# Optimization experiments

Measured on AMD Instinct MI355X. Metric: run time of the kernel, lower is better.

The kernel has to match this reference:

```python
import jax, jax.numpy as jnp
import numpy as np

EPS_PROJ = 0.004   # float32 branch of _project
EPS_MIN = 1e-15


def _poincare_linear(x, weight_v, weight_g, bias, c):
    c = c.reshape(())
    rc = jnp.sqrt(c)
    # z_unit: column-normalized weight (weight_v / ||weight_v||_col)
    z_unit = weight_v / jnp.maximum(jnp.linalg.norm(weight_v, axis=0), EPS_MIN)  # [in, out]
    # unidirectional Poincare MLR
    drcr = 2.0 * rc * bias                                  # [out]
    rcx = rc * x                                            # [N, in]
    cx2 = jnp.sum(rcx * rcx, axis=-1, keepdims=True)        # [N, 1]
    num = 2.0 * (rcx @ z_unit) * jnp.cosh(drcr) - (1.0 + cx2) * jnp.sinh(drcr)
    mlr = 2.0 * weight_g / rc * jnp.arcsinh(num / jnp.maximum(1.0 - cx2, EPS_MIN))  # [N, out]
    # map back to the ball: sinh, then gyro-half map
    y = jnp.sinh(rc * mlr) / rc
    y = y / (1.0 + jnp.sqrt(1.0 + c * jnp.sum(y * y, axis=-1, keepdims=True)))
    # _project onto ball of curvature k = -c
    k = -c
    maxnorm = (1.0 - EPS_PROJ) / jnp.sqrt(jnp.maximum(jnp.abs(k), EPS_MIN))
    maxnorm = jnp.where(k < 0, maxnorm, jnp.float32(1e15))
    norm = jnp.maximum(jnp.linalg.norm(y, axis=-1, keepdims=True), EPS_MIN)
    return jnp.where(norm > maxnorm, y / norm * maxnorm, y)


def setup_inputs() -> dict:
    key = jax.random.key(0)
    k1, k2, k3 = jax.random.split(key, 3)
    N, IN, OUT = 32768, 1024, 1024
    # points strictly inside the unit Poincare ball (||x|| ~ 0.64)
    x = jax.random.normal(k1, (N, IN), dtype=jnp.float32) * 0.02
    std = (2.0 * IN * OUT) ** (-0.5)
    weight_v = jax.random.normal(k2, (IN, OUT), dtype=jnp.float32) * std
    weight_g = jax.random.uniform(k3, (OUT,), dtype=jnp.float32, minval=0.5, maxval=1.5) * std * (IN ** 0.5)
    bias = jnp.zeros((OUT,), dtype=jnp.float32)
    c = jnp.ones((1,), dtype=jnp.float32)
    return {"x": x, "weight_v": weight_v, "weight_g": weight_g, "bias": bias, "c": c}


def reference(x, weight_v, weight_g, bias, c):
    return _poincare_linear(x, weight_v, weight_g, bias, c)
```

## Files before the change

kernel.cpp:

```cpp
#include <hip/hip_runtime.h>

#define K_DIM 1024
#define N_DIM 1024

typedef short v8s __attribute__((ext_vector_type(8)));
typedef float v4f __attribute__((ext_vector_type(4)));

__device__ __forceinline__ unsigned int bf16_rne(float f) {
    unsigned int u = __float_as_uint(f);
    u += 0x7FFFu + ((u >> 16) & 1u);
    return u >> 16;
}

__global__ void sumsq_cols(const float* __restrict__ wv, float* __restrict__ colss) {
    __shared__ float red[4][64];
    const int t = threadIdx.x;
    const int cj = t & 63, rr = t >> 6;
    const int col = (blockIdx.x & 15) * 64 + cj;
    const int k0 = (blockIdx.x >> 4) * 128 + rr * 32;
    float ss = 0.f;
#pragma unroll 8
    for (int i = 0; i < 32; ++i) {
        float v = wv[(size_t)(k0 + i) * N_DIM + col];
        ss = fmaf(v, v, ss);
    }
    red[rr][cj] = ss;
    __syncthreads();
    if (rr == 0) atomicAdd(&colss[col], red[0][cj] + red[1][cj] + red[2][cj] + red[3][cj]);
}

__global__ void finalize_cols(const float* __restrict__ colss, const float* __restrict__ wg,
                              const float* __restrict__ bias, const float* __restrict__ cptr,
                              float* __restrict__ colinv, float* __restrict__ coshd,
                              float* __restrict__ sinhd, float* __restrict__ gfac) {
    const int col = blockIdx.x * 256 + threadIdx.x;
    const float rc = sqrtf(cptr[0]);
    colinv[col] = 1.0f / fmaxf(sqrtf(colss[col]), 1e-15f);
    float d = 2.0f * rc * bias[col];
    float e = __expf(d), ie = 1.0f / e;
    coshd[col] = 0.5f * (e + ie);
    sinhd[col] = 0.5f * (e - ie);
    gfac[col] = 2.0f * wg[col];
}

__global__ void build_bt(const float* __restrict__ wv, const float* __restrict__ colinv,
                         unsigned short* __restrict__ Btf) {
    __shared__ float tile[64 * 65];
    const int t = threadIdx.x;
    const int ti = blockIdx.x & 15;
    const int tj = blockIdx.x >> 4;
    {
        const int kl = t >> 2;
        const int cc = t & 3;
        const float* src = wv + (size_t)(ti * 64 + kl) * N_DIM + tj * 64 + cc * 16;
        float4 fq[4];
#pragma unroll
        for (int i = 0; i < 4; ++i) fq[i] = ((const float4*)src)[i];
        float* dst = &tile[kl * 65 + cc * 16];
#pragma unroll
        for (int i = 0; i < 4; ++i) {
            dst[4 * i + 0] = fq[i].x; dst[4 * i + 1] = fq[i].y;
            dst[4 * i + 2] = fq[i].z; dst[4 * i + 3] = fq[i].w;
        }
    }
    __syncthreads();
    {
        const int nl = t & 63, kc = t >> 6;
        const int n = tj * 64 + nl;
        const float ci = colinv[n];
        const int nt_g = tj * 4 + (nl >> 4);
#pragma unroll
        for (int h = 0; h < 2; ++h) {
            const int k8g = ti * 8 + kc * 2 + h;
            const int ks_g = k8g >> 2;
            const int L = (nl & 15) | ((k8g & 3) << 4);
            unsigned int p[4];
#pragma unroll
            for (int j = 0; j < 4; ++j) {
                float v0 = tile[(kc * 16 + h * 8 + 2 * j) * 65 + nl] * ci;
                float v1 = tile[(kc * 16 + h * 8 + 2 * j + 1) * 65 + nl] * ci;
                p[j] = bf16_rne(v0) | (bf16_rne(v1) << 16);
            }
            *(uint4*)(Btf + ((size_t)(nt_g * 32 + ks_g) * 64 + L) * 8) =
                make_uint4(p[0], p[1], p[2], p[3]);
        }
    }
}

__global__ void prep_a(const float* __restrict__ x, unsigned short* __restrict__ Axf,
                       float* __restrict__ rowss) {
    __shared__ float xs[16 * 1028];
    const int t = threadIdx.x;
    const int b = blockIdx.x;
    {
        const int r = t >> 4;
        const int c = t & 15;
        const float* xp = x + (size_t)(b * 16 + r) * K_DIM + c * 4;
        float* dst = &xs[r * 1028 + c * 4];
        float ss = 0.f;
#pragma unroll
        for (int it = 0; it < 16; ++it) {
            float4 v = *(const float4*)(xp + it * 64);
            ss = fmaf(v.x, v.x, ss); ss = fmaf(v.y, v.y, ss);
            ss = fmaf(v.z, v.z, ss); ss = fmaf(v.w, v.w, ss);
            *(float4*)(dst + it * 64) = v;
        }
        ss += __shfl_xor(ss, 1); ss += __shfl_xor(ss, 2);
        ss += __shfl_xor(ss, 4); ss += __shfl_xor(ss, 8);
        if (c == 0) rowss[b * 16 + r] = ss;
    }
    __syncthreads();
    {
        const int w = t >> 6, L = t & 63;
        const int lm = L & 15, q = L >> 4;
#pragma unroll
        for (int i = 0; i < 8; ++i) {
            const int ks = w * 8 + i;
            const float* src = &xs[lm * 1028 + ks * 32 + q * 8];
            float4 f0 = *(const float4*)(src);
            float4 f1 = *(const float4*)(src + 4);
            float vals[8] = {f0.x, f0.y, f0.z, f0.w, f1.x, f1.y, f1.z, f1.w};
            unsigned int p[4];
#pragma unroll
            for (int j = 0; j < 4; ++j)
                p[j] = bf16_rne(vals[2 * j]) | (bf16_rne(vals[2 * j + 1]) << 16);
            *(uint4*)(Axf + ((size_t)b * 32 + ks) * 512 + L * 8) =
                make_uint4(p[0], p[1], p[2], p[3]);
        }
    }
}

__launch_bounds__(512, 2)
__global__ void gemm_fused(const unsigned short* __restrict__ Axf,
                           const unsigned short* __restrict__ Btf,
                           const float* __restrict__ rowss, const float* __restrict__ cptr,
                           const float* __restrict__ coshd, const float* __restrict__ sinhd,
                           const float* __restrict__ gfac,
                           float* __restrict__ out) {
    __shared__ __align__(16) unsigned short As[4 * 32 * 512];

    const int t = threadIdx.x;
    const int w = t >> 6, L = t & 63;
    const int lm = L & 15, q = L >> 4;
    const int bm = blockIdx.x;
    const int r0 = bm * 64;

    const unsigned short* ag = Axf + (size_t)bm * 65536;
#pragma unroll
    for (int r = 0; r < 16; ++r) {
        __builtin_amdgcn_global_load_lds(
            (const __attribute__((address_space(1))) unsigned int*)(ag + r * 4096 + t * 8),
            (__attribute__((address_space(3))) unsigned int*)(As + r * 4096 + t * 8),
            16, 0, 0);
    }

    const unsigned short* bw = Btf + (size_t)(w * 8) * 32 * 512 + (size_t)L * 8;

    v4f acc[4][8];
#pragma unroll
    for (int i = 0; i < 4; ++i)
#pragma unroll
        for (int j = 0; j < 8; ++j) acc[i][j] = (v4f){0.f, 0.f, 0.f, 0.f};

    v8s bA[8], bB[8];
#pragma unroll
    for (int n = 0; n < 8; ++n)
        bA[n] = *(const v8s*)(bw + (n * 32) * 512);

    __syncthreads();

    const unsigned short* asw = As + L * 8;

#pragma unroll 1
    for (int kp = 0; kp < 16; ++kp) {
        const int k0 = kp * 2;
#pragma unroll
        for (int n = 0; n < 8; ++n)
            bB[n] = *(const v8s*)(bw + (n * 32 + k0 + 1) * 512);
        {
            v8s a[4];
#pragma unroll
            for (int mt = 0; mt < 4; ++mt)
                a[mt] = *(const v8s*)(asw + (mt * 32 + k0) * 512);
            __builtin_amdgcn_s_setprio(1);
#pragma unroll
            for (int mt = 0; mt < 4; ++mt)
#pragma unroll
                for (int n = 0; n < 8; ++n)
                    acc[mt][n] = __builtin_amdgcn_mfma_f32_16x16x32_bf16(
                        a[mt], bA[n], acc[mt][n], 0, 0, 0);
            __builtin_amdgcn_s_setprio(0);
        }
        if (kp < 15) {
#pragma unroll
            for (int n = 0; n < 8; ++n)
                bA[n] = *(const v8s*)(bw + (n * 32 + k0 + 2) * 512);
        }
        {
            v8s a[4];
#pragma unroll
            for (int mt = 0; mt < 4; ++mt)
                a[mt] = *(const v8s*)(asw + (mt * 32 + k0 + 1) * 512);
            __builtin_amdgcn_s_setprio(1);
#pragma unroll
            for (int mt = 0; mt < 4; ++mt)
#pragma unroll
                for (int n = 0; n < 8; ++n)
                    acc[mt][n] = __builtin_amdgcn_mfma_f32_16x16x32_bf16(
                        a[mt], bB[n], acc[mt][n], 0, 0, 0);
            __builtin_amdgcn_s_setprio(0);
        }
    }

    float* s_rsum = (float*)As;

    const float cc = cptr[0];
    const float rc = sqrtf(cc);
    const float two_rc = 2.0f * rc;
    const float halfinvrc = 0.5f / rc;
    float ch[8], sh[8], gf[8];
#pragma unroll
    for (int n = 0; n < 8; ++n) {
        const int col = w * 128 + n * 16 + lm;
        ch[n] = coshd[col]; sh[n] = sinhd[col]; gf[n] = gfac[col];
    }

    __syncthreads();
    if (t < 64) s_rsum[t] = 0.f;
    __syncthreads();

#pragma unroll
    for (int mt = 0; mt < 4; ++mt) {
        const int mloc = mt * 16 + q * 4;
        float sx[4];
#pragma unroll
        for (int rr = 0; rr < 4; ++rr) sx[rr] = cc * rowss[r0 + mloc + rr];
        float rs[4] = {0.f, 0.f, 0.f, 0.f};
#pragma unroll
        for (int n = 0; n < 8; ++n) {
            v4f d = acc[mt][n];
#pragma unroll
            for (int rr = 0; rr < 4; ++rr) {
                float cx2 = sx[rr];
                float num = two_rc * d[rr] * ch[n] - (1.0f + cx2) * sh[n];
                float den = fmaxf(1.0f - cx2, 1e-15f);
                float tt = num * __builtin_amdgcn_rcpf(den);
                float as_ = __logf(fabsf(tt) + sqrtf(fmaf(tt, tt, 1.0f)));
                as_ = copysignf(as_, tt);
                float u = gf[n] * as_;
                float e = __expf(u);
                float y = (e - __builtin_amdgcn_rcpf(e)) * halfinvrc;
                d[rr] = y;
                rs[rr] = fmaf(y, y, rs[rr]);
            }
            acc[mt][n] = d;
        }
#pragma unroll
        for (int rr = 0; rr < 4; ++rr) {
            float v = rs[rr];
            v += __shfl_xor(v, 1); v += __shfl_xor(v, 2);
            v += __shfl_xor(v, 4); v += __shfl_xor(v, 8);
            if (lm == 0) atomicAdd(&s_rsum[mloc + rr], v);
        }
    }
    __syncthreads();

    const float mn = (cc > 0.f) ? 0.996f / sqrtf(fmaxf(cc, 1e-15f)) : 1e15f;
#pragma unroll
    for (int mt = 0; mt < 4; ++mt) {
        const int mloc = mt * 16 + q * 4;
        float f[4];
#pragma unroll
        for (int rr = 0; rr < 4; ++rr) {
            const float s = s_rsum[mloc + rr];
            const float scale = 1.0f / (1.0f + sqrtf(fmaf(cc, s, 1.0f)));
            const float nrm = fmaxf(sqrtf(s) * scale, 1e-15f);
            f[rr] = scale * (nrm > mn ? mn / nrm : 1.0f);
        }
#pragma unroll
        for (int rr = 0; rr < 4; ++rr) {
            float* op = out + (size_t)(r0 + mloc + rr) * N_DIM + w * 128 + lm;
#pragma unroll
            for (int n = 0; n < 8; ++n) op[n * 16] = acc[mt][n][rr] * f[rr];
        }
    }
}

__launch_bounds__(256, 3)
__global__ void gemm_phase(const float* __restrict__ x, const unsigned short* __restrict__ Btf,
                           const float* __restrict__ cptr, const float* __restrict__ coshd,
                           const float* __restrict__ sinhd, const float* __restrict__ gfac,
                           float* __restrict__ out, float* __restrict__ rowsum) {
    __shared__ __align__(16) unsigned short As[16 * 512];
    __shared__ __align__(16) unsigned short Bs[16 * 512];
    __shared__ float s_cx2[128];
    __shared__ float s_rsum[128];

    const int t = threadIdx.x;
    const int w = t >> 6, L = t & 63;
    const int lm = L & 15, q = L >> 4;
    const int bn = blockIdx.x & 7;
    const int bm = blockIdx.x >> 3;
    const int r0 = bm * 128;

    if (t < 128) { s_cx2[t] = 0.f; s_rsum[t] = 0.f; }

    v4f acc[16];
#pragma unroll
    for (int i = 0; i < 16; ++i) acc[i] = (v4f){0.f, 0.f, 0.f, 0.f};

    const int smt0 = w * 2;
    const float* xr0 = x + (size_t)(r0 + smt0 * 16 + lm) * K_DIM;
    const float* xr1 = xr0 + (size_t)16 * K_DIM;
    float xp0 = 0.f, xp1 = 0.f;
    const int wm = w & 1, wn = w >> 1;

    for (int kq = 0; kq < 16; ++kq) {
        const int kbase = kq * 64;
#pragma unroll
        for (int i = 0; i < 4; ++i) {
            const int nt = smt0 + (i & 1);
            const int ks = i >> 1;
            const unsigned short* gp =
                Btf + ((size_t)((bn * 8 + nt) * 32 + (kq * 2 + ks)) * 64 + L) * 8;
            __builtin_amdgcn_global_load_lds(
                (const __attribute__((address_space(1))) unsigned int*)gp,
                (__attribute__((address_space(3))) unsigned int*)&Bs[(nt * 2 + ks) * 512],
                16, 0, 0);
        }
#pragma unroll
        for (int i = 0; i < 4; ++i) {
            const int half = i & 1;
            const int ks = i >> 1;
            const float* xr = half ? xr1 : xr0;
            const int kg = kbase + ks * 32 + q * 8;
            float4 f0 = *(const float4*)(xr + kg);
            float4 f1 = *(const float4*)(xr + kg + 4);
            float vals[8] = {f0.x, f0.y, f0.z, f0.w, f1.x, f1.y, f1.z, f1.w};
            unsigned int pk[4];
            float ssl = 0.f;
#pragma unroll
            for (int j = 0; j < 4; ++j) {
                ssl = fmaf(vals[2 * j], vals[2 * j], ssl);
                ssl = fmaf(vals[2 * j + 1], vals[2 * j + 1], ssl);
                pk[j] = bf16_rne(vals[2 * j]) | (bf16_rne(vals[2 * j + 1]) << 16);
            }
            if (half) xp1 += ssl; else xp0 += ssl;
            *(uint4*)&As[((smt0 + half) * 2 + ks) * 512 + L * 8] =
                make_uint4(pk[0], pk[1], pk[2], pk[3]);
        }
        __syncthreads();
#pragma unroll
        for (int ks = 0; ks < 2; ++ks) {
            v8s a[4], b[4];
#pragma unroll
            for (int mi = 0; mi < 4; ++mi)
                a[mi] = *(const v8s*)&As[((wm * 4 + mi) * 2 + ks) * 512 + L * 8];
#pragma unroll
            for (int ni = 0; ni < 4; ++ni)
                b[ni] = *(const v8s*)&Bs[((wn * 4 + ni) * 2 + ks) * 512 + L * 8];
#pragma unroll
            for (int mi = 0; mi < 4; ++mi)
#pragma unroll
                for (int ni = 0; ni < 4; ++ni)
                    acc[mi * 4 + ni] = __builtin_amdgcn_mfma_f32_16x16x32_bf16(
                        a[mi], b[ni], acc[mi * 4 + ni], 0, 0, 0);
        }
        __syncthreads();
    }

    atomicAdd(&s_cx2[smt0 * 16 + lm], xp0);
    atomicAdd(&s_cx2[smt0 * 16 + 16 + lm], xp1);
    __syncthreads();

    const float cc = cptr[0];
    const float rc = sqrtf(cc);
    const float two_rc = 2.0f * rc;
    const float halfinvrc = 0.5f / rc;
    float ch[4], sh[4], gf[4];
#pragma unroll
    for (int ni = 0; ni < 4; ++ni) {
        const int n = bn * 128 + wn * 64 + ni * 16 + lm;
        ch[ni] = coshd[n]; sh[ni] = sinhd[n]; gf[ni] = gfac[n];
    }
#pragma unroll
    for (int mi = 0; mi < 4; ++mi) {
        const int mloc = wm * 64 + mi * 16 + q * 4;
        float sx[4];
#pragma unroll
        for (int rr = 0; rr < 4; ++rr) sx[rr] = cc * s_cx2[mloc + rr];
        float rs[4] = {0.f, 0.f, 0.f, 0.f};
#pragma unroll
        for (int ni = 0; ni < 4; ++ni) {
            v4f d = acc[mi * 4 + ni];
#pragma unroll
            for (int rr = 0; rr < 4; ++rr) {
                float cx2 = sx[rr];
                float num = two_rc * d[rr] * ch[ni] - (1.0f + cx2) * sh[ni];
                float den = fmaxf(1.0f - cx2, 1e-15f);
                float tt = num * __builtin_amdgcn_rcpf(den);
                float as_ = __logf(fabsf(tt) + sqrtf(fmaf(tt, tt, 1.0f)));
                as_ = copysignf(as_, tt);
                float u = gf[ni] * as_;
                float e = __expf(u);
                float y = (e - __builtin_amdgcn_rcpf(e)) * halfinvrc;
                d[rr] = y;
                rs[rr] = fmaf(y, y, rs[rr]);
            }
            acc[mi * 4 + ni] = d;
        }
#pragma unroll
        for (int rr = 0; rr < 4; ++rr) {
            float v = rs[rr];
            v += __shfl_xor(v, 1); v += __shfl_xor(v, 2);
            v += __shfl_xor(v, 4); v += __shfl_xor(v, 8);
            if (lm == 0) atomicAdd(&s_rsum[mloc + rr], v);
        }
#pragma unroll
        for (int rr = 0; rr < 4; ++rr) {
            const int row = r0 + mloc + rr;
            float* op = out + (size_t)row * N_DIM + bn * 128 + wn * 64 + lm;
#pragma unroll
            for (int ni = 0; ni < 4; ++ni) op[ni * 16] = acc[mi * 4 + ni][rr];
        }
    }
    __syncthreads();
    if (t < 128) atomicAdd(&rowsum[r0 + t], s_rsum[t]);
}

__global__ void rescale(float* __restrict__ out, const float* __restrict__ rowsum,
                        const float* __restrict__ cptr) {
    const int t = threadIdx.x;
    const int row = blockIdx.x * 4 + (t >> 6);
    const float cc = cptr[0];
    const float s = rowsum[row];
    const float scale = 1.0f / (1.0f + sqrtf(fmaf(cc, s, 1.0f)));
    const float nrm = fmaxf(sqrtf(s) * scale, 1e-15f);
    const float mn = (cc > 0.f) ? 0.996f / sqrtf(fmaxf(cc, 1e-15f)) : 1e15f;
    const float f = scale * (nrm > mn ? mn / nrm : 1.0f);
    float4* p = (float4*)(out + (size_t)row * N_DIM) + (t & 63);
#pragma unroll
    for (int j = 0; j < 4; ++j) {
        float4 v = p[j * 64];
        v.x *= f; v.y *= f; v.z *= f; v.w *= f;
        p[j * 64] = v;
    }
}

extern "C" void kernel_launch(void* const* d_in, const int* in_sizes, int n_in,
                              void* d_out, int out_size, void* d_ws, size_t ws_size,
                              hipStream_t stream) {
    const float* x    = (const float*)d_in[0];
    const float* wv   = (const float*)d_in[1];
    const float* wg   = (const float*)d_in[2];
    const float* bias = (const float*)d_in[3];
    const float* cptr = (const float*)d_in[4];
    float* out = (float*)d_out;

    const int OUT = in_sizes[2];
    const int IN  = in_sizes[1] / OUT;
    const int M   = in_sizes[0] / IN;

    float* colss  = (float*)d_ws;
    float* rowsum = colss + 1024;
    float* rowss  = rowsum + M;
    float* colinv = rowss + M;
    float* coshd  = colinv + 1024;
    float* sinhd  = coshd + 1024;
    float* gfac   = sinhd + 1024;
    unsigned short* Btf = (unsigned short*)(gfac + 1024);
    unsigned short* Axf = Btf + (size_t)IN * OUT;

    const size_t need = (size_t)(1024 + 2 * M + 4096) * 4 + (size_t)IN * OUT * 2
                      + (size_t)M * IN * 2;

    hipMemsetAsync(colss, 0, 1024 * sizeof(float), stream);
    sumsq_cols<<<128, 256, 0, stream>>>(wv, colss);
    finalize_cols<<<OUT / 256, 256, 0, stream>>>(colss, wg, bias, cptr, colinv, coshd, sinhd, gfac);
    build_bt<<<(IN / 64) * (OUT / 64), 256, 0, stream>>>(wv, colinv, Btf);
    if (ws_size >= need) {
        prep_a<<<M / 16, 256, 0, stream>>>(x, Axf, rowss);
        gemm_fused<<<M / 64, 512, 0, stream>>>(
            Axf, Btf, rowss, cptr, coshd, sinhd, gfac, out);
    } else {
        hipMemsetAsync(rowsum, 0, (size_t)M * sizeof(float), stream);
        gemm_phase<<<(M / 128) * (OUT / 128), 256, 0, stream>>>(
            x, Btf, cptr, coshd, sinhd, gfac, out, rowsum);
        rescale<<<M / 4, 256, 0, stream>>>(out, rowsum, cptr);
    }
}
```

Baseline: 362.3 us.

## Fuse x bf16 conversion into persistent GEMM and merge weight prep kernels

Drops the separate prep_a pass that wrote a bf16 copy of x to global memory. The GEMM becomes a persistent kernel over 256 blocks that converts each 64-row x panel to bf16 straight into an XOR-swizzled LDS layout, accumulating row sums of squares in shared memory. The next panel's staging overlaps with the current panel's epilogue. The three weight-prep kernels (column norms, finalize, transpose) merge into one prep_w kernel that recomputes column sums per block, which adds redundant reads of weight_v. The fallback path, memsets and global atomics are removed.

```diff
diff --git a/kernel.cpp b/kernel.cpp
--- a/kernel.cpp
+++ b/kernel.cpp
@@ -2,6 +2,7 @@
 
 #define K_DIM 1024
 #define N_DIM 1024
+#define GRID 256
 
 typedef short v8s __attribute__((ext_vector_type(8)));
 typedef float v4f __attribute__((ext_vector_type(4)));
@@ -12,51 +13,34 @@
     return u >> 16;
 }
 
-__global__ void sumsq_cols(const float* __restrict__ wv, float* __restrict__ colss) {
-    __shared__ float red[4][64];
-    const int t = threadIdx.x;
-    const int cj = t & 63, rr = t >> 6;
-    const int col = (blockIdx.x & 15) * 64 + cj;
-    const int k0 = (blockIdx.x >> 4) * 128 + rr * 32;
-    float ss = 0.f;
-#pragma unroll 8
-    for (int i = 0; i < 32; ++i) {
-        float v = wv[(size_t)(k0 + i) * N_DIM + col];
-        ss = fmaf(v, v, ss);
-    }
-    red[rr][cj] = ss;
-    __syncthreads();
-    if (rr == 0) atomicAdd(&colss[col], red[0][cj] + red[1][cj] + red[2][cj] + red[3][cj]);
-}
-
-__global__ void finalize_cols(const float* __restrict__ colss, const float* __restrict__ wg,
-                              const float* __restrict__ bias, const float* __restrict__ cptr,
-                              float* __restrict__ colinv, float* __restrict__ coshd,
-                              float* __restrict__ sinhd, float* __restrict__ gfac) {
-    const int col = blockIdx.x * 256 + threadIdx.x;
-    const float rc = sqrtf(cptr[0]);
-    colinv[col] = 1.0f / fmaxf(sqrtf(colss[col]), 1e-15f);
-    float d = 2.0f * rc * bias[col];
-    float e = __expf(d), ie = 1.0f / e;
-    coshd[col] = 0.5f * (e + ie);
-    sinhd[col] = 0.5f * (e - ie);
-    gfac[col] = 2.0f * wg[col];
-}
-
-__global__ void build_bt(const float* __restrict__ wv, const float* __restrict__ colinv,
-                         unsigned short* __restrict__ Btf) {
+__global__ void prep_w(const float* __restrict__ wv, const float* __restrict__ wg,
+                       const float* __restrict__ bias, const float* __restrict__ cptr,
+                       float* __restrict__ coshd, float* __restrict__ sinhd,
+                       float* __restrict__ gfac, unsigned short* __restrict__ Btf) {
     __shared__ float tile[64 * 65];
+    __shared__ float cred[4][64];
+    __shared__ float cinv[64];
     const int t = threadIdx.x;
     const int ti = blockIdx.x & 15;
     const int tj = blockIdx.x >> 4;
     {
-        const int kl = t >> 2;
-        const int cc = t & 3;
-        const float* src = wv + (size_t)(ti * 64 + kl) * N_DIM + tj * 64 + cc * 16;
+        const int cj = t & 63, rg = t >> 6;
+        const float* wp = wv + (size_t)(rg * 256) * N_DIM + tj * 64 + cj;
+        float ss = 0.f;
+#pragma unroll 4
+        for (int r = 0; r < 256; ++r) {
+            float v = wp[(size_t)r * N_DIM];
+            ss = fmaf(v, v, ss);
+        }
+        cred[rg][cj] = ss;
+    }
+    {
+        const int kl = t >> 2, cq = t & 3;
+        const float* src = wv + (size_t)(ti * 64 + kl) * N_DIM + tj * 64 + cq * 16;
         float4 fq[4];
 #pragma unroll
         for (int i = 0; i < 4; ++i) fq[i] = ((const float4*)src)[i];
-        float* dst = &tile[kl * 65 + cc * 16];
+        float* dst = &tile[kl * 65 + cq * 16];
 #pragma unroll
         for (int i = 0; i < 4; ++i) {
             dst[4 * i + 0] = fq[i].x; dst[4 * i + 1] = fq[i].y;
@@ -64,10 +48,23 @@
         }
     }
     __syncthreads();
+    if (t < 64) {
+        float s = cred[0][t] + cred[1][t] + cred[2][t] + cred[3][t];
+        cinv[t] = 1.0f / fmaxf(sqrtf(s), 1e-15f);
+        if (ti == 0) {
+            const int col = tj * 64 + t;
+            const float rc = sqrtf(cptr[0]);
+            float d = 2.0f * rc * bias[col];
+            float e = __expf(d), ie = 1.0f / e;
+            coshd[col] = 0.5f * (e + ie);
+            sinhd[col] = 0.5f * (e - ie);
+            gfac[col] = 2.0f * wg[col];
+        }
+    }
+    __syncthreads();
     {
         const int nl = t & 63, kc = t >> 6;
-        const int n = tj * 64 + nl;
-        const float ci = colinv[n];
+        const float ci = cinv[nl];
         const int nt_g = tj * 4 + (nl >> 4);
 #pragma unroll
         for (int h = 0; h < 2; ++h) {
@@ -87,137 +84,55 @@
     }
 }
 
-__global__ void prep_a(const float* __restrict__ x, unsigned short* __restrict__ Axf,
-                       float* __restrict__ rowss) {
-    __shared__ float xs[16 * 1028];
-    const int t = threadIdx.x;
-    const int b = blockIdx.x;
-    {
-        const int r = t >> 4;
-        const int c = t & 15;
-        const float* xp = x + (size_t)(b * 16 + r) * K_DIM + c * 4;
-        float* dst = &xs[r * 1028 + c * 4];
+__device__ __forceinline__ void stage_panel(const float* __restrict__ xp,
+                                            unsigned short* __restrict__ Asl,
+                                            float* __restrict__ rowssbuf, int t) {
+#pragma unroll 2
+    for (int it = 0; it < 16; ++it) {
+        const int g = it * 512 + t;
+        const int row = g >> 7, k8 = g & 127;
+        const float4* fp = (const float4*)xp + (size_t)g * 2;
+        float4 f0 = fp[0];
+        float4 f1 = fp[1];
+        float vals[8] = {f0.x, f0.y, f0.z, f0.w, f1.x, f1.y, f1.z, f1.w};
+        unsigned int p[4];
         float ss = 0.f;
 #pragma unroll
-        for (int it = 0; it < 16; ++it) {
-            float4 v = *(const float4*)(xp + it * 64);
-            ss = fmaf(v.x, v.x, ss); ss = fmaf(v.y, v.y, ss);
-            ss = fmaf(v.z, v.z, ss); ss = fmaf(v.w, v.w, ss);
-            *(float4*)(dst + it * 64) = v;
-        }
-        ss += __shfl_xor(ss, 1); ss += __shfl_xor(ss, 2);
-        ss += __shfl_xor(ss, 4); ss += __shfl_xor(ss, 8);
-        if (c == 0) rowss[b * 16 + r] = ss;
-    }
-    __syncthreads();
-    {
-        const int w = t >> 6, L = t & 63;
-        const int lm = L & 15, q = L >> 4;
-#pragma unroll
-        for (int i = 0; i < 8; ++i) {
-            const int ks = w * 8 + i;
-            const float* src = &xs[lm * 1028 + ks * 32 + q * 8];
-            float4 f0 = *(const float4*)(src);
-            float4 f1 = *(const float4*)(src + 4);
-            float vals[8] = {f0.x, f0.y, f0.z, f0.w, f1.x, f1.y, f1.z, f1.w};
-            unsigned int p[4];
-#pragma unroll
-            for (int j = 0; j < 4; ++j)
-                p[j] = bf16_rne(vals[2 * j]) | (bf16_rne(vals[2 * j + 1]) << 16);
-            *(uint4*)(Axf + ((size_t)b * 32 + ks) * 512 + L * 8) =
-                make_uint4(p[0], p[1], p[2], p[3]);
-        }
+        for (int j = 0; j < 4; ++j) {
+            ss = fmaf(vals[2 * j], vals[2 * j], ss);
+            ss = fmaf(vals[2 * j + 1], vals[2 * j + 1], ss);
+            p[j] = bf16_rne(vals[2 * j]) | (bf16_rne(vals[2 * j + 1]) << 16);
+        }
+        ss += __shfl_xor(ss, 1);  ss += __shfl_xor(ss, 2);  ss += __shfl_xor(ss, 4);
+        ss += __shfl_xor(ss, 8);  ss += __shfl_xor(ss, 16); ss += __shfl_xor(ss, 32);
+        if ((t & 63) == 0) atomicAdd(&rowssbuf[row], ss);
+        const int mt = row >> 4, lm2 = row & 15, ks = k8 >> 2, qq = k8 & 3;
+        const int idx = ((mt * 32 + ks) * 512) + (((lm2 ^ (ks & 7)) | (qq << 4)) * 8);
+        *(uint4*)&Asl[idx] = make_uint4(p[0], p[1], p[2], p[3]);
     }
 }
 
 __launch_bounds__(512, 2)
-__global__ void gemm_fused(const unsigned short* __restrict__ Axf,
+__global__ void gemm_fused(const float* __restrict__ x,
                            const unsigned short* __restrict__ Btf,
-                           const float* __restrict__ rowss, const float* __restrict__ cptr,
+                           const float* __restrict__ cptr,
                            const float* __restrict__ coshd, const float* __restrict__ sinhd,
                            const float* __restrict__ gfac,
-                           float* __restrict__ out) {
+                           float* __restrict__ out, int panels) {
     __shared__ __align__(16) unsigned short As[4 * 32 * 512];
+    __shared__ float s_rowss[2][64];
+    __shared__ float s_rsum[64];
 
     const int t = threadIdx.x;
     const int w = t >> 6, L = t & 63;
     const int lm = L & 15, q = L >> 4;
     const int bm = blockIdx.x;
-    const int r0 = bm * 64;
-
-    const unsigned short* ag = Axf + (size_t)bm * 65536;
-#pragma unroll
-    for (int r = 0; r < 16; ++r) {
-        __builtin_amdgcn_global_load_lds(
-            (const __attribute__((address_space(1))) unsigned int*)(ag + r * 4096 + t * 8),
-            (__attribute__((address_space(3))) unsigned int*)(As + r * 4096 + t * 8),
-            16, 0, 0);
-    }
-
-    const unsigned short* bw = Btf + (size_t)(w * 8) * 32 * 512 + (size_t)L * 8;
-
-    v4f acc[4][8];
-#pragma unroll
-    for (int i = 0; i < 4; ++i)
-#pragma unroll
-        for (int j = 0; j < 8; ++j) acc[i][j] = (v4f){0.f, 0.f, 0.f, 0.f};
-
-    v8s bA[8], bB[8];
-#pragma unroll
-    for (int n = 0; n < 8; ++n)
-        bA[n] = *(const v8s*)(bw + (n * 32) * 512);
-
-    __syncthreads();
-
-    const unsigned short* asw = As + L * 8;
-
-#pragma unroll 1
-    for (int kp = 0; kp < 16; ++kp) {
-        const int k0 = kp * 2;
-#pragma unroll
-        for (int n = 0; n < 8; ++n)
-            bB[n] = *(const v8s*)(bw + (n * 32 + k0 + 1) * 512);
-        {
-            v8s a[4];
-#pragma unroll
-            for (int mt = 0; mt < 4; ++mt)
-                a[mt] = *(const v8s*)(asw + (mt * 32 + k0) * 512);
-            __builtin_amdgcn_s_setprio(1);
-#pragma unroll
-            for (int mt = 0; mt < 4; ++mt)
-#pragma unroll
-                for (int n = 0; n < 8; ++n)
-                    acc[mt][n] = __builtin_amdgcn_mfma_f32_16x16x32_bf16(
-                        a[mt], bA[n], acc[mt][n], 0, 0, 0);
-            __builtin_amdgcn_s_setprio(0);
-        }
-        if (kp < 15) {
-#pragma unroll
-            for (int n = 0; n < 8; ++n)
-                bA[n] = *(const v8s*)(bw + (n * 32 + k0 + 2) * 512);
-        }
-        {
-            v8s a[4];
-#pragma unroll
-            for (int mt = 0; mt < 4; ++mt)
-                a[mt] = *(const v8s*)(asw + (mt * 32 + k0 + 1) * 512);
-            __builtin_amdgcn_s_setprio(1);
-#pragma unroll
-            for (int mt = 0; mt < 4; ++mt)
-#pragma unroll
-                for (int n = 0; n < 8; ++n)
-                    acc[mt][n] = __builtin_amdgcn_mfma_f32_16x16x32_bf16(
-                        a[mt], bB[n], acc[mt][n], 0, 0, 0);
-            __builtin_amdgcn_s_setprio(0);
-        }
-    }
-
-    float* s_rsum = (float*)As;
 
     const float cc = cptr[0];
     const float rc = sqrtf(cc);
     const float two_rc = 2.0f * rc;
     const float halfinvrc = 0.5f / rc;
+    const float mn = (cc > 0.f) ? 0.996f / sqrtf(fmaxf(cc, 1e-15f)) : 1e15f;
     float ch[8], sh[8], gf[8];
 #pragma unroll
     for (int n = 0; n < 8; ++n) {
@@ -225,225 +140,134 @@
         ch[n] = coshd[col]; sh[n] = sinhd[col]; gf[n] = gfac[col];
     }
 
+    const unsigned short* bw = Btf + (size_t)(w * 8) * 32 * 512 + (size_t)L * 8;
+
+    if (t < 64) s_rowss[0][t] = 0.f;
     __syncthreads();
-    if (t < 64) s_rsum[t] = 0.f;
-    __syncthreads();
-
-#pragma unroll
-    for (int mt = 0; mt < 4; ++mt) {
-        const int mloc = mt * 16 + q * 4;
-        float sx[4];
-#pragma unroll
-        for (int rr = 0; rr < 4; ++rr) sx[rr] = cc * rowss[r0 + mloc + rr];
-        float rs[4] = {0.f, 0.f, 0.f, 0.f};
-#pragma unroll
-        for (int n = 0; n < 8; ++n) {
-            v4f d = acc[mt][n];
+    stage_panel(x + (size_t)bm * 64 * K_DIM, As, s_rowss[0], t);
+
+#pragma unroll 1
+    for (int i = 0; i < panels; ++i) {
+        const int p = bm + i * GRID;
+        const int pb = i & 1, nb = pb ^ 1;
+        const bool more = (i + 1 < panels);
+        __syncthreads();
+
+        v4f acc[4][8];
+#pragma unroll
+        for (int a = 0; a < 4; ++a)
+#pragma unroll
+            for (int b = 0; b < 8; ++b) acc[a][b] = (v4f){0.f, 0.f, 0.f, 0.f};
+
+        v8s bA[8], bB[8];
+#pragma unroll
+        for (int n = 0; n < 8; ++n)
+            bA[n] = *(const v8s*)(bw + (n * 32) * 512);
+
+#pragma unroll 1
+        for (int kp = 0; kp < 16; ++kp) {
+            const int k0 = kp * 2;
+#pragma unroll
+            for (int n = 0; n < 8; ++n)
+                bB[n] = *(const v8s*)(bw + (n * 32 + k0 + 1) * 512);
+            {
+                const int lx = ((lm ^ (k0 & 7)) | (q << 4)) * 8;
+                v8s a[4];
+#pragma unroll
+                for (int mt = 0; mt < 4; ++mt)
+                    a[mt] = *(const v8s*)&As[(mt * 32 + k0) * 512 + lx];
+                __builtin_amdgcn_s_setprio(1);
+#pragma unroll
+                for (int mt = 0; mt < 4; ++mt)
+#pragma unroll
+                    for (int n = 0; n < 8; ++n)
+                        acc[mt][n] = __builtin_amdgcn_mfma_f32_16x16x32_bf16(
+                            a[mt], bA[n], acc[mt][n], 0, 0, 0);
+                __builtin_amdgcn_s_setprio(0);
+            }
+            if (kp < 15) {
+#pragma unroll
+                for (int n = 0; n < 8; ++n)
+                    bA[n] = *(const v8s*)(bw + (n * 32 + k0 + 2) * 512);
+            }
+            {
+                const int lx = ((lm ^ ((k0 + 1) & 7)) | (q << 4)) * 8;
+                v8s a[4];
+#pragma unroll
+                for (int mt = 0; mt < 4; ++mt)
+                    a[mt] = *(const v8s*)&As[(mt * 32 + k0 + 1) * 512 + lx];
+                __builtin_amdgcn_s_setprio(1);
+#pragma unroll
+                for (int mt = 0; mt < 4; ++mt)
+#pragma unroll
+                    for (int n = 0; n < 8; ++n)
+                        acc[mt][n] = __builtin_amdgcn_mfma_f32_16x16x32_bf16(
+                            a[mt], bB[n], acc[mt][n], 0, 0, 0);
+                __builtin_amdgcn_s_setprio(0);
+            }
+        }
+
+        __syncthreads();
+        if (t < 64) { s_rsum[t] = 0.f; if (more) s_rowss[nb][t] = 0.f; }
+        __syncthreads();
+
+        if (more) stage_panel(x + (size_t)(p + GRID) * 64 * K_DIM, As, s_rowss[nb], t);
+
+        const float* rb = s_rowss[pb];
+#pragma unroll
+        for (int mt = 0; mt < 4; ++mt) {
+            const int mloc = mt * 16 + q * 4;
+            float sx[4];
+#pragma unroll
+            for (int rr = 0; rr < 4; ++rr) sx[rr] = cc * rb[mloc + rr];
+            float rs[4] = {0.f, 0.f, 0.f, 0.f};
+#pragma unroll
+            for (int n = 0; n < 8; ++n) {
+                v4f d = acc[mt][n];
+#pragma unroll
+                for (int rr = 0; rr < 4; ++rr) {
+                    float cx2 = sx[rr];
+                    float num = two_rc * d[rr] * ch[n] - (1.0f + cx2) * sh[n];
+                    float den = fmaxf(1.0f - cx2, 1e-15f);
+                    float tt = num * __builtin_amdgcn_rcpf(den);
+                    float as_ = __logf(fabsf(tt) + sqrtf(fmaf(tt, tt, 1.0f)));
+                    as_ = copysignf(as_, tt);
+                    float u = gf[n] * as_;
+                    float e = __expf(u);
+                    float y = (e - __builtin_amdgcn_rcpf(e)) * halfinvrc;
+                    d[rr] = y;
+                    rs[rr] = fmaf(y, y, rs[rr]);
+                }
+                acc[mt][n] = d;
+            }
 #pragma unroll
             for (int rr = 0; rr < 4; ++rr) {
-                float cx2 = sx[rr];
-                float num = two_rc * d[rr] * ch[n] - (1.0f + cx2) * sh[n];
-                float den = fmaxf(1.0f - cx2, 1e-15f);
-                float tt = num * __builtin_amdgcn_rcpf(den);
-                float as_ = __logf(fabsf(tt) + sqrtf(fmaf(tt, tt, 1.0f)));
-                as_ = copysignf(as_, tt);
-                float u = gf[n] * as_;
-                float e = __expf(u);
-                float y = (e - __builtin_amdgcn_rcpf(e)) * halfinvrc;
-                d[rr] = y;
-                rs[rr] = fmaf(y, y, rs[rr]);
-            }
-            acc[mt][n] = d;
-        }
-#pragma unroll
-        for (int rr = 0; rr < 4; ++rr) {
-            float v = rs[rr];
-            v += __shfl_xor(v, 1); v += __shfl_xor(v, 2);
-            v += __shfl_xor(v, 4); v += __shfl_xor(v, 8);
-            if (lm == 0) atomicAdd(&s_rsum[mloc + rr], v);
-        }
-    }
-    __syncthreads();
-
-    const float mn = (cc > 0.f) ? 0.996f / sqrtf(fmaxf(cc, 1e-15f)) : 1e15f;
-#pragma unroll
-    for (int mt = 0; mt < 4; ++mt) {
-        const int mloc = mt * 16 + q * 4;
-        float f[4];
-#pragma unroll
-        for (int rr = 0; rr < 4; ++rr) {
-            const float s = s_rsum[mloc + rr];
-            const float scale = 1.0f / (1.0f + sqrtf(fmaf(cc, s, 1.0f)));
-            const float nrm = fmaxf(sqrtf(s) * scale, 1e-15f);
-            f[rr] = scale * (nrm > mn ? mn / nrm : 1.0f);
-        }
-#pragma unroll
-        for (int rr = 0; rr < 4; ++rr) {
-            float* op = out + (size_t)(r0 + mloc + rr) * N_DIM + w * 128 + lm;
-#pragma unroll
-            for (int n = 0; n < 8; ++n) op[n * 16] = acc[mt][n][rr] * f[rr];
-        }
-    }
-}
-
-__launch_bounds__(256, 3)
-__global__ void gemm_phase(const float* __restrict__ x, const unsigned short* __restrict__ Btf,
-                           const float* __restrict__ cptr, const float* __restrict__ coshd,
-                           const float* __restrict__ sinhd, const float* __restrict__ gfac,
-                           float* __restrict__ out, float* __restrict__ rowsum) {
-    __shared__ __align__(16) unsigned short As[16 * 512];
-    __shared__ __align__(16) unsigned short Bs[16 * 512];
-    __shared__ float s_cx2[128];
-    __shared__ float s_rsum[128];
-
-    const int t = threadIdx.x;
-    const int w = t >> 6, L = t & 63;
-    const int lm = L & 15, q = L >> 4;
-    const int bn = blockIdx.x & 7;
-    const int bm = blockIdx.x >> 3;
-    const int r0 = bm * 128;
-
-    if (t < 128) { s_cx2[t] = 0.f; s_rsum[t] = 0.f; }
-
-    v4f acc[16];
-#pragma unroll
-    for (int i = 0; i < 16; ++i) acc[i] = (v4f){0.f, 0.f, 0.f, 0.f};
-
-    const int smt0 = w * 2;
-    const float* xr0 = x + (size_t)(r0 + smt0 * 16 + lm) * K_DIM;
-    const float* xr1 = xr0 + (size_t)16 * K_DIM;
-    float xp0 = 0.f, xp1 = 0.f;
-    const int wm = w & 1, wn = w >> 1;
-
-    for (int kq = 0; kq < 16; ++kq) {
-        const int kbase = kq * 64;
-#pragma unroll
-        for (int i = 0; i < 4; ++i) {
-            const int nt = smt0 + (i & 1);
-            const int ks = i >> 1;
-            const unsigned short* gp =
-                Btf + ((size_t)((bn * 8 + nt) * 32 + (kq * 2 + ks)) * 64 + L) * 8;
-            __builtin_amdgcn_global_load_lds(
-                (const __attribute__((address_space(1))) unsigned int*)gp,
-                (__attribute__((address_space(3))) unsigned int*)&Bs[(nt * 2 + ks) * 512],
-                16, 0, 0);
-        }
-#pragma unroll
-        for (int i = 0; i < 4; ++i) {
-            const int half = i & 1;
-            const int ks = i >> 1;
-            const float* xr = half ? xr1 : xr0;
-            const int kg = kbase + ks * 32 + q * 8;
-            float4 f0 = *(const float4*)(xr + kg);
-            float4 f1 = *(const float4*)(xr + kg + 4);
-            float vals[8] = {f0.x, f0.y, f0.z, f0.w, f1.x, f1.y, f1.z, f1.w};
-            unsigned int pk[4];
-            float ssl = 0.f;
-#pragma unroll
-            for (int j = 0; j < 4; ++j) {
-                ssl = fmaf(vals[2 * j], vals[2 * j], ssl);
-                ssl = fmaf(vals[2 * j + 1], vals[2 * j + 1], ssl);
-                pk[j] = bf16_rne(vals[2 * j]) | (bf16_rne(vals[2 * j + 1]) << 16);
-            }
-            if (half) xp1 += ssl; else xp0 += ssl;
-            *(uint4*)&As[((smt0 + half) * 2 + ks) * 512 + L * 8] =
-                make_uint4(pk[0], pk[1], pk[2], pk[3]);
-        }
-        __syncthreads();
-#pragma unroll
-        for (int ks = 0; ks < 2; ++ks) {
-            v8s a[4], b[4];
-#pragma unroll
-            for (int mi = 0; mi < 4; ++mi)
-                a[mi] = *(const v8s*)&As[((wm * 4 + mi) * 2 + ks) * 512 + L * 8];
-#pragma unroll
-            for (int ni = 0; ni < 4; ++ni)
-                b[ni] = *(const v8s*)&Bs[((wn * 4 + ni) * 2 + ks) * 512 + L * 8];
-#pragma unroll
-            for (int mi = 0; mi < 4; ++mi)
-#pragma unroll
-                for (int ni = 0; ni < 4; ++ni)
-                    acc[mi * 4 + ni] = __builtin_amdgcn_mfma_f32_16x16x32_bf16(
-                        a[mi], b[ni], acc[mi * 4 + ni], 0, 0, 0);
-        }
-        __syncthreads();
-    }
-
-    atomicAdd(&s_cx2[smt0 * 16 + lm], xp0);
-    atomicAdd(&s_cx2[smt0 * 16 + 16 + lm], xp1);
-    __syncthreads();
-
-    const float cc = cptr[0];
-    const float rc = sqrtf(cc);
-    const float two_rc = 2.0f * rc;
-    const float halfinvrc = 0.5f / rc;
-    float ch[4], sh[4], gf[4];
-#pragma unroll
-    for (int ni = 0; ni < 4; ++ni) {
-        const int n = bn * 128 + wn * 64 + ni * 16 + lm;
-        ch[ni] = coshd[n]; sh[ni] = sinhd[n]; gf[ni] = gfac[n];
-    }
-#pragma unroll
-    for (int mi = 0; mi < 4; ++mi) {
-        const int mloc = wm * 64 + mi * 16 + q * 4;
-        float sx[4];
-#pragma unroll
-        for (int rr = 0; rr < 4; ++rr) sx[rr] = cc * s_cx2[mloc + rr];
-        float rs[4] = {0.f, 0.f, 0.f, 0.f};
-#pragma unroll
-        for (int ni = 0; ni < 4; ++ni) {
-            v4f d = acc[mi * 4 + ni];
+                float v = rs[rr];
+                v += __shfl_xor(v, 1); v += __shfl_xor(v, 2);
+                v += __shfl_xor(v, 4); v += __shfl_xor(v, 8);
+                if (lm == 0) atomicAdd(&s_rsum[mloc + rr], v);
+            }
+        }
+        __syncthreads();
+
+#pragma unroll
+        for (int mt = 0; mt < 4; ++mt) {
+            const int mloc = mt * 16 + q * 4;
+            float f[4];
 #pragma unroll
             for (int rr = 0; rr < 4; ++rr) {
-                float cx2 = sx[rr];
-                float num = two_rc * d[rr] * ch[ni] - (1.0f + cx2) * sh[ni];
-                float den = fmaxf(1.0f - cx2, 1e-15f);
-                float tt = num * __builtin_amdgcn_rcpf(den);
-                float as_ = __logf(fabsf(tt) + sqrtf(fmaf(tt, tt, 1.0f)));
-                as_ = copysignf(as_, tt);
-                float u = gf[ni] * as_;
-                float e = __expf(u);
-                float y = (e - __builtin_amdgcn_rcpf(e)) * halfinvrc;
-                d[rr] = y;
-                rs[rr] = fmaf(y, y, rs[rr]);
-            }
-            acc[mi * 4 + ni] = d;
-        }
-#pragma unroll
-        for (int rr = 0; rr < 4; ++rr) {
-            float v = rs[rr];
-            v += __shfl_xor(v, 1); v += __shfl_xor(v, 2);
-            v += __shfl_xor(v, 4); v += __shfl_xor(v, 8);
-            if (lm == 0) atomicAdd(&s_rsum[mloc + rr], v);
-        }
-#pragma unroll
-        for (int rr = 0; rr < 4; ++rr) {
-            const int row = r0 + mloc + rr;
-            float* op = out + (size_t)row * N_DIM + bn * 128 + wn * 64 + lm;
-#pragma unroll
-            for (int ni = 0; ni < 4; ++ni) op[ni * 16] = acc[mi * 4 + ni][rr];
-        }
-    }
-    __syncthreads();
-    if (t < 128) atomicAdd(&rowsum[r0 + t], s_rsum[t]);
-}
-
-__global__ void rescale(float* __restrict__ out, const float* __restrict__ rowsum,
-                        const float* __restrict__ cptr) {
-    const int t = threadIdx.x;
-    const int row = blockIdx.x * 4 + (t >> 6);
-    const float cc = cptr[0];
-    const float s = rowsum[row];
-    const float scale = 1.0f / (1.0f + sqrtf(fmaf(cc, s, 1.0f)));
-    const float nrm = fmaxf(sqrtf(s) * scale, 1e-15f);
-    const float mn = (cc > 0.f) ? 0.996f / sqrtf(fmaxf(cc, 1e-15f)) : 1e15f;
-    const float f = scale * (nrm > mn ? mn / nrm : 1.0f);
-    float4* p = (float4*)(out + (size_t)row * N_DIM) + (t & 63);
-#pragma unroll
-    for (int j = 0; j < 4; ++j) {
-        float4 v = p[j * 64];
-        v.x *= f; v.y *= f; v.z *= f; v.w *= f;
-        p[j * 64] = v;
+                const float s = s_rsum[mloc + rr];
+                const float scale = 1.0f / (1.0f + sqrtf(fmaf(cc, s, 1.0f)));
+                const float nrm = fmaxf(sqrtf(s) * scale, 1e-15f);
+                f[rr] = scale * (nrm > mn ? mn / nrm : 1.0f);
+            }
+#pragma unroll
+            for (int rr = 0; rr < 4; ++rr) {
+                float* op = out + (size_t)(p * 64 + mloc + rr) * N_DIM + w * 128 + lm;
+#pragma unroll
+                for (int n = 0; n < 8; ++n) op[n * 16] = acc[mt][n][rr] * f[rr];
+            }
+        }
     }
 }
 
@@ -461,31 +285,15 @@
     const int IN  = in_sizes[1] / OUT;
     const int M   = in_sizes[0] / IN;
 
-    float* colss  = (float*)d_ws;
-    float* rowsum = colss + 1024;
-    float* rowss  = rowsum + M;
-    float* colinv = rowss + M;
-    float* coshd  = colinv + 1024;
-    float* sinhd  = coshd + 1024;
-    float* gfac   = sinhd + 1024;
+    float* coshd = (float*)d_ws;
+    float* sinhd = coshd + 1024;
+    float* gfac  = sinhd + 1024;
     unsigned short* Btf = (unsigned short*)(gfac + 1024);
-    unsigned short* Axf = Btf + (size_t)IN * OUT;
-
-    const size_t need = (size_t)(1024 + 2 * M + 4096) * 4 + (size_t)IN * OUT * 2
-                      + (size_t)M * IN * 2;
-
-    hipMemsetAsync(colss, 0, 1024 * sizeof(float), stream);
-    sumsq_cols<<<128, 256, 0, stream>>>(wv, colss);
-    finalize_cols<<<OUT / 256, 256, 0, stream>>>(colss, wg, bias, cptr, colinv, coshd, sinhd, gfac);
-    build_bt<<<(IN / 64) * (OUT / 64), 256, 0, stream>>>(wv, colinv, Btf);
-    if (ws_size >= need) {
-        prep_a<<<M / 16, 256, 0, stream>>>(x, Axf, rowss);
-        gemm_fused<<<M / 64, 512, 0, stream>>>(
-            Axf, Btf, rowss, cptr, coshd, sinhd, gfac, out);
-    } else {
-        hipMemsetAsync(rowsum, 0, (size_t)M * sizeof(float), stream);
-        gemm_phase<<<(M / 128) * (OUT / 128), 256, 0, stream>>>(
-            x, Btf, cptr, coshd, sinhd, gfac, out, rowsum);
-        rescale<<<M / 4, 256, 0, stream>>>(out, rowsum, cptr);
-    }
-}
+
+    prep_w<<<(IN / 64) * (OUT / 64), 256, 0, stream>>>(
+        wv, wg, bias, cptr, coshd, sinhd, gfac, Btf);
+
+    const int panels = (M / 64) / GRID;
+    gemm_fused<<<GRID, 512, 0, stream>>>(
+        x, Btf, cptr, coshd, sinhd, gfac, out, panels);
+}
```

New measurement: 371.0 us. 1.02x slower.
